# Optimization experiments

Hardware: AMD Instinct MI355X
Metric: run time of the kernel (lower is better)

Reference implementation:

```python
import jax, jax.numpy as jnp
import numpy as np

NEG_SLOPE = 0.2    # DenseGATConv attention leaky_relu slope (PyG default)
ACT_SLOPE = 0.01   # block activation LeakyReLU slope
HEADS = 3


def setup_inputs() -> dict:
    key = jax.random.key(0)
    B, N, D0, D1, D2, H = 512, 128, 128, 64, 64, HEADS
    ks = jax.random.split(key, 7)
    x = jax.random.normal(ks[0], (B * N, D0), jnp.float32)
    # equal-sized graphs: sorted graph ids, N atoms per graph
    batch_mask = jnp.repeat(jnp.arange(B, dtype=jnp.int32), N)
    s0 = 1.0 / np.sqrt(D0)
    s1 = 1.0 / np.sqrt(D1)
    s2 = 1.0 / np.sqrt(D2)
    W1 = jax.random.normal(ks[1], (D0, H * D1), jnp.float32) * s0
    att_src1 = jax.random.normal(ks[2], (H, D1), jnp.float32) * s1
    att_dst1 = jax.random.normal(ks[3], (H, D1), jnp.float32) * s1
    b1 = jnp.zeros((D1,), jnp.float32)
    W2 = jax.random.normal(ks[4], (D1, H * D2), jnp.float32) * s1
    att_src2 = jax.random.normal(ks[5], (H, D2), jnp.float32) * s2
    att_dst2 = jax.random.normal(ks[6], (H, D2), jnp.float32) * s2
    b2 = jnp.zeros((D2,), jnp.float32)
    return dict(x=x, batch_mask=batch_mask, W1=W1, att_src1=att_src1,
                att_dst1=att_dst1, b1=b1, W2=W2, att_src2=att_src2,
                att_dst2=att_dst2, b2=b2, batch_size=B, n_max=N)


def _dense_gat(x, adj, W, a_src, a_dst, b):
    # x: [B, N, Din], adj: [B, N, N] (self-loops already set). concat=False.
    B, N, _ = x.shape
    H, C = a_src.shape
    h = (x @ W).reshape(B, N, H, C)                       # lin (no bias)
    a_s = jnp.einsum('bnhc,hc->bnh', h, a_src)            # per-node src score
    a_d = jnp.einsum('bnhc,hc->bnh', h, a_dst)            # per-node dst score
    alpha = a_s[:, None, :, :] + a_d[:, :, None, :]       # [B, i, j, H]
    alpha = jax.nn.leaky_relu(alpha, NEG_SLOPE)
    alpha = jnp.where(adj[..., None] == 0, -jnp.inf, alpha)
    alpha = jax.nn.softmax(alpha, axis=2)                 # over source j
    out = jnp.einsum('bijh,bjhc->bihc', alpha, h)         # [B, N, H, C]
    return out.mean(axis=2) + b                           # concat=False -> head mean


def reference(x, batch_mask, W1, att_src1, att_dst1, b1,
              W2, att_src2, att_dst2, b2, batch_size, n_max):
    total, D0 = x.shape
    counts = jnp.bincount(batch_mask, length=batch_size)          # atoms per graph
    starts = jnp.cumsum(counts) - counts
    pos = jnp.arange(total) - starts[batch_mask]                  # slot within graph
    # to_dense_batch
    xd = jnp.zeros((batch_size, n_max, D0), x.dtype).at[batch_mask, pos].set(x)
    node_in = jnp.arange(n_max)[None, :] < counts[:, None]        # [B, N] valid mask
    # block adjacency: fully connected within each graph, diag zeroed...
    adj = (node_in[:, :, None] & node_in[:, None, :]).astype(x.dtype)
    # ...then DenseGATConv add_loop=True re-sets the full diagonal to 1
    adj = jnp.where(jnp.eye(n_max, dtype=bool), jnp.asarray(1.0, x.dtype), adj)
    h = _dense_gat(xd, adj, W1, att_src1, att_dst1, b1)
    h = jax.nn.leaky_relu(h, ACT_SLOPE)
    h = _dense_gat(h, adj, W2, att_src2, att_dst2, b2)
    h = jax.nn.leaky_relu(h, ACT_SLOPE)
    return jnp.sum(h, axis=1)                                     # sum pooling -> [B, D2]
```

## Files before the change

### kernel.cpp

```cpp
#include <hip/hip_runtime.h>
#include <stdint.h>

#define NROW 128
#define HCC  192

typedef __attribute__((ext_vector_type(8))) __bf16 bf16x8;
typedef __attribute__((ext_vector_type(4))) float  f32x4;

static __device__ __forceinline__ uint16_t f2bf(float f) {
    union { float f; uint32_t i; } v; v.f = f;
    uint32_t x = v.i;
    return (uint16_t)((x + 0x7FFFu + ((x >> 16) & 1u)) >> 16);
}
static __device__ __forceinline__ uint32_t pk2bf(float a, float b) {
    union { __bf16 h[2]; uint32_t u; } pk;
    pk.h[0] = (__bf16)a; pk.h[1] = (__bf16)b;
    return pk.u;
}

__global__ __launch_bounds__(256)
void prep_kernel(const float* __restrict__ W1, const float* __restrict__ W2,
                 uint16_t* __restrict__ wT1, uint16_t* __restrict__ wT2)
{
    int bid = blockIdx.x, t = threadIdx.x;
    if (bid < 96) {
        int idx = bid * 256 + t;
        int c = idx >> 7, k = idx & 127;
        wT1[c * 128 + k] = f2bf(W1[k * HCC + c]);
    } else {
        int idx = (bid - 96) * 256 + t;
        int c = idx >> 6, k = idx & 63;
        wT2[c * 64 + k] = f2bf(W2[k * HCC + c]);
    }
}

template<int K, bool POOL>
__global__ __launch_bounds__(512, 4)
void layer_kernel(const void* __restrict__ xin, const uint16_t* __restrict__ wTg,
                  const float* __restrict__ att_src, const float* __restrict__ att_dst,
                  const float* __restrict__ bias, void* __restrict__ outp)
{
    constexpr int XS = K + 8;
    constexpr int HS = 136;
    __shared__ __align__(16) uint16_t buf[HCC * HS];
    __shared__ __align__(16) float as_s[3 * 128];
    __shared__ __align__(16) float ad_s[3 * 128];
    __shared__ float attS[HCC], attD[HCC], bia[64], pool_s[8 * 64];

    uint16_t* wTl = buf;
    uint16_t* hT  = buf;

    const int b = blockIdx.x, t = threadIdx.x;
    const int w = t >> 6, l = t & 63, lr = l & 15, lg = l >> 4;
    const int i0 = w * 16;

    bf16x8 afr[K / 32];
    float4 raw[K == 128 ? 8 : 1][2];
    if (K == 128) {
        const float* xg = (const float*)xin + ((long)b * NROW + i0 + lr) * 128;
#pragma unroll
        for (int q = 0; q < 4; ++q) {
            raw[q][0] = *(const float4*)(xg + q * 32 + lg * 8);
            raw[q][1] = *(const float4*)(xg + q * 32 + lg * 8 + 4);
        }
    } else {
        const uint16_t* xg = (const uint16_t*)xin + ((long)b * NROW + i0 + lr) * 64;
#pragma unroll
        for (int q = 0; q < 2; ++q)
            afr[q] = *(const bf16x8*)(xg + q * 32 + lg * 8);
    }

    {
        constexpr int CH = K / 8;
#pragma unroll
        for (int p = 0; p < HCC * CH / 512; ++p) {
            int idx = t + p * 512; int row = idx / CH; int c8 = (idx % CH) * 8;
            *(uint4*)&wTl[row * XS + c8] = *(const uint4*)(wTg + row * K + c8);
        }
    }
    if (t < HCC) attS[t] = att_src[t];
    else if (t < 2 * HCC) attD[t - HCC] = att_dst[t - HCC];
    else if (t < 2 * HCC + 64) bia[t - 2 * HCC] = bias[t - 2 * HCC];

    if (K == 128) {
#pragma unroll
        for (int q = 0; q < 4; ++q) {
            bf16x8 a;
            a[0] = (__bf16)raw[q][0].x; a[1] = (__bf16)raw[q][0].y;
            a[2] = (__bf16)raw[q][0].z; a[3] = (__bf16)raw[q][0].w;
            a[4] = (__bf16)raw[q][1].x; a[5] = (__bf16)raw[q][1].y;
            a[6] = (__bf16)raw[q][1].z; a[7] = (__bf16)raw[q][1].w;
            afr[q] = a;
        }
    }
    __syncthreads();

    f32x4 hacc[12];
#pragma unroll
    for (int f = 0; f < 12; ++f) hacc[f] = (f32x4){0.f, 0.f, 0.f, 0.f};
#pragma unroll
    for (int q = 0; q < K / 32; ++q) {
        bf16x8 af = afr[q];
#pragma unroll
        for (int f = 0; f < 12; ++f) {
            bf16x8 bf = *(const bf16x8*)&wTl[(f * 16 + lr) * XS + q * 32 + lg * 8];
            hacc[f] = __builtin_amdgcn_mfma_f32_16x16x32_bf16(af, bf, hacc[f], 0, 0, 0);
        }
    }
    __syncthreads();

    {
        float ps[12], pd[12];
#pragma unroll
        for (int q = 0; q < 12; ++q) { ps[q] = 0.f; pd[q] = 0.f; }
#pragma unroll
        for (int f = 0; f < 12; ++f) {
            int hd = f >> 2;
            float av = attS[f * 16 + lr], dv = attD[f * 16 + lr];
#pragma unroll
            for (int r = 0; r < 4; ++r) {
                float hv = hacc[f][r];
                ps[hd * 4 + r] += hv * av;
                pd[hd * 4 + r] += hv * dv;
            }
        }
#pragma unroll
        for (int off = 1; off < 16; off <<= 1)
#pragma unroll
            for (int q = 0; q < 12; ++q) {
                ps[q] += __shfl_xor(ps[q], off);
                pd[q] += __shfl_xor(pd[q], off);
            }
        if (lr == 0) {
#pragma unroll
            for (int hd = 0; hd < 3; ++hd)
#pragma unroll
                for (int r = 0; r < 4; ++r) {
                    as_s[hd * 128 + i0 + lg * 4 + r] = ps[hd * 4 + r];
                    ad_s[hd * 128 + i0 + lg * 4 + r] = pd[hd * 4 + r];
                }
        }
#pragma unroll
        for (int f = 0; f < 12; ++f) {
            uint2 pv = make_uint2(pk2bf(hacc[f][0], hacc[f][1]),
                                  pk2bf(hacc[f][2], hacc[f][3]));
            *(uint2*)&hT[(f * 16 + lr) * HS + i0 + lg * 4] = pv;
        }
    }
    __syncthreads();

    f32x4 oacc[4];
#pragma unroll
    for (int f = 0; f < 4; ++f) oacc[f] = (f32x4){0.f, 0.f, 0.f, 0.f};

    for (int hd = 0; hd < 3; ++hd) {
        float a0 = as_s[hd * 128 + l], a1 = as_s[hd * 128 + l + 64];
        float mx = fmaxf(a0, a1);
#pragma unroll
        for (int off = 1; off < 64; off <<= 1) mx = fmaxf(mx, __shfl_xor(mx, off));
        float ad = ad_s[hd * 128 + i0 + lr];
        float m0 = mx + ad;
        float mi = fmaxf(m0, 0.2f * m0);

        float e[4][8];
        float zp = 0.f;
#pragma unroll
        for (int q = 0; q < 4; ++q) {
            float4 s0 = *(const float4*)&as_s[hd * 128 + q * 32 + lg * 8];
            float4 s1 = *(const float4*)&as_s[hd * 128 + q * 32 + lg * 8 + 4];
            float sv[8] = {s0.x, s0.y, s0.z, s0.w, s1.x, s1.y, s1.z, s1.w};
#pragma unroll
            for (int m = 0; m < 8; ++m) {
                float tt = sv[m] + ad;
                tt = fmaxf(tt, 0.2f * tt);
                float ev = __expf(tt - mi);
                e[q][m] = ev; zp += ev;
            }
        }
        zp += __shfl_xor(zp, 16);
        zp += __shfl_xor(zp, 32);
        float inv = 1.0f / zp;
        bf16x8 ap[4];
#pragma unroll
        for (int q = 0; q < 4; ++q)
#pragma unroll
            for (int m = 0; m < 8; ++m) ap[q][m] = (__bf16)(e[q][m] * inv);
#pragma unroll
        for (int q = 0; q < 4; ++q)
#pragma unroll
            for (int f = 0; f < 4; ++f) {
                bf16x8 bf = *(const bf16x8*)&hT[(hd * 64 + f * 16 + lr) * HS + q * 32 + lg * 8];
                oacc[f] = __builtin_amdgcn_mfma_f32_16x16x32_bf16(ap[q], bf, oacc[f], 0, 0, 0);
            }
    }

    const float inv3 = 1.f / 3.f;
    if (!POOL) {
        uint16_t* x2 = (uint16_t*)outp + (long)b * NROW * 64;
#pragma unroll
        for (int f = 0; f < 4; ++f) {
            int c = f * 16 + lr;
            float bv = bia[c];
#pragma unroll
            for (int r = 0; r < 4; ++r) {
                int i = i0 + lg * 4 + r;
                float v = oacc[f][r] * inv3 + bv;
                v = fmaxf(v, 0.01f * v);
                x2[i * 64 + c] = f2bf(v);
            }
        }
    } else {
#pragma unroll
        for (int f = 0; f < 4; ++f) {
            int c = f * 16 + lr;
            float bv = bia[c];
            float s = 0.f;
#pragma unroll
            for (int r = 0; r < 4; ++r) {
                float v = oacc[f][r] * inv3 + bv;
                v = fmaxf(v, 0.01f * v);
                s += v;
            }
            s += __shfl_xor(s, 16);
            s += __shfl_xor(s, 32);
            if (lg == 0) pool_s[w * 64 + c] = s;
        }
        __syncthreads();
        if (t < 64) {
            float s = 0.f;
#pragma unroll
            for (int q = 0; q < 8; ++q) s += pool_s[q * 64 + t];
            ((float*)outp)[(long)b * 64 + t] = s;
        }
    }
}

extern "C" void kernel_launch(void* const* d_in, const int* in_sizes, int n_in,
                              void* d_out, int out_size, void* d_ws, size_t ws_size,
                              hipStream_t stream)
{
    const float* x   = (const float*)d_in[0];
    const float* W1  = (const float*)d_in[2];
    const float* as1 = (const float*)d_in[3];
    const float* ad1 = (const float*)d_in[4];
    const float* b1  = (const float*)d_in[5];
    const float* W2  = (const float*)d_in[6];
    const float* as2 = (const float*)d_in[7];
    const float* ad2 = (const float*)d_in[8];
    const float* b2  = (const float*)d_in[9];

    uint16_t* wT1 = (uint16_t*)d_ws;
    uint16_t* wT2 = wT1 + 192 * 128;
    uint16_t* x2  = wT2 + 192 * 64;

    prep_kernel<<<144, 256, 0, stream>>>(W1, W2, wT1, wT2);
    layer_kernel<128, false><<<512, 512, 0, stream>>>((const void*)x,  wT1, as1, ad1, b1, (void*)x2);
    layer_kernel<64,  true ><<<512, 512, 0, stream>>>((const void*)x2, wT2, as2, ad2, b2, d_out);
}
```

Baseline: 138.3 us.

## Fuse both GAT layers into one kernel keeping intermediate features in LDS

Merges the two per-layer kernels into a single kernel per graph. The layer-1 output stays in shared memory as bf16 and never makes a global round trip. Layer-2 weights are prefetched into registers during the layer-1 softmax. The per-head max reductions are also batched across heads. This removes one launch and the intermediate global write and read, at the cost of more register pressure and a longer single kernel.

```diff
diff --git a/kernel.cpp b/kernel.cpp
--- a/kernel.cpp
+++ b/kernel.cpp
@@ -12,10 +12,9 @@
     uint32_t x = v.i;
     return (uint16_t)((x + 0x7FFFu + ((x >> 16) & 1u)) >> 16);
 }
-static __device__ __forceinline__ uint32_t pk2bf(float a, float b) {
-    union { __bf16 h[2]; uint32_t u; } pk;
-    pk.h[0] = (__bf16)a; pk.h[1] = (__bf16)b;
-    return pk.u;
+static __device__ __forceinline__ uint16_t bfbits(float f) {
+    __bf16 h = (__bf16)f;
+    union { __bf16 h; uint16_t u; } c; c.h = h; return c.u;
 }
 
 __global__ __launch_bounds__(256)
@@ -34,132 +33,73 @@
     }
 }
 
-template<int K, bool POOL>
-__global__ __launch_bounds__(512, 4)
-void layer_kernel(const void* __restrict__ xin, const uint16_t* __restrict__ wTg,
-                  const float* __restrict__ att_src, const float* __restrict__ att_dst,
-                  const float* __restrict__ bias, void* __restrict__ outp)
-{
-    constexpr int XS = K + 8;
-    constexpr int HS = 136;
-    __shared__ __align__(16) uint16_t buf[HCC * HS];
-    __shared__ __align__(16) float as_s[3 * 128];
-    __shared__ __align__(16) float ad_s[3 * 128];
-    __shared__ float attS[HCC], attD[HCC], bia[64], pool_s[8 * 64];
-
-    uint16_t* wTl = buf;
-    uint16_t* hT  = buf;
-
-    const int b = blockIdx.x, t = threadIdx.x;
-    const int w = t >> 6, l = t & 63, lr = l & 15, lg = l >> 4;
-    const int i0 = w * 16;
-
-    bf16x8 afr[K / 32];
-    float4 raw[K == 128 ? 8 : 1][2];
-    if (K == 128) {
-        const float* xg = (const float*)xin + ((long)b * NROW + i0 + lr) * 128;
-#pragma unroll
-        for (int q = 0; q < 4; ++q) {
-            raw[q][0] = *(const float4*)(xg + q * 32 + lg * 8);
-            raw[q][1] = *(const float4*)(xg + q * 32 + lg * 8 + 4);
-        }
-    } else {
-        const uint16_t* xg = (const uint16_t*)xin + ((long)b * NROW + i0 + lr) * 64;
-#pragma unroll
-        for (int q = 0; q < 2; ++q)
-            afr[q] = *(const bf16x8*)(xg + q * 32 + lg * 8);
-    }
-
-    {
-        constexpr int CH = K / 8;
-#pragma unroll
-        for (int p = 0; p < HCC * CH / 512; ++p) {
-            int idx = t + p * 512; int row = idx / CH; int c8 = (idx % CH) * 8;
-            *(uint4*)&wTl[row * XS + c8] = *(const uint4*)(wTg + row * K + c8);
-        }
-    }
-    if (t < HCC) attS[t] = att_src[t];
-    else if (t < 2 * HCC) attD[t - HCC] = att_dst[t - HCC];
-    else if (t < 2 * HCC + 64) bia[t - 2 * HCC] = bias[t - 2 * HCC];
-
-    if (K == 128) {
-#pragma unroll
-        for (int q = 0; q < 4; ++q) {
-            bf16x8 a;
-            a[0] = (__bf16)raw[q][0].x; a[1] = (__bf16)raw[q][0].y;
-            a[2] = (__bf16)raw[q][0].z; a[3] = (__bf16)raw[q][0].w;
-            a[4] = (__bf16)raw[q][1].x; a[5] = (__bf16)raw[q][1].y;
-            a[6] = (__bf16)raw[q][1].z; a[7] = (__bf16)raw[q][1].w;
-            afr[q] = a;
-        }
-    }
-    __syncthreads();
-
-    f32x4 hacc[12];
-#pragma unroll
-    for (int f = 0; f < 12; ++f) hacc[f] = (f32x4){0.f, 0.f, 0.f, 0.f};
-#pragma unroll
-    for (int q = 0; q < K / 32; ++q) {
-        bf16x8 af = afr[q];
-#pragma unroll
-        for (int f = 0; f < 12; ++f) {
-            bf16x8 bf = *(const bf16x8*)&wTl[(f * 16 + lr) * XS + q * 32 + lg * 8];
-            hacc[f] = __builtin_amdgcn_mfma_f32_16x16x32_bf16(af, bf, hacc[f], 0, 0, 0);
-        }
-    }
-    __syncthreads();
-
-    {
-        float ps[12], pd[12];
-#pragma unroll
-        for (int q = 0; q < 12; ++q) { ps[q] = 0.f; pd[q] = 0.f; }
-#pragma unroll
-        for (int f = 0; f < 12; ++f) {
-            int hd = f >> 2;
-            float av = attS[f * 16 + lr], dv = attD[f * 16 + lr];
+#define HS 136
+#define S2 72
+
+static __device__ __forceinline__
+void scores_and_hT(const f32x4* hacc, const float* attS, const float* attD,
+                   uint16_t* hT, float* as_s, float* ad_s,
+                   int i0, int lr, int lg)
+{
+    float ps[12], pd[12];
+#pragma unroll
+    for (int q = 0; q < 12; ++q) { ps[q] = 0.f; pd[q] = 0.f; }
+#pragma unroll
+    for (int f = 0; f < 12; ++f) {
+        int hd = f >> 2;
+        float av = attS[f * 16 + lr], dv = attD[f * 16 + lr];
+#pragma unroll
+        for (int r = 0; r < 4; ++r) {
+            float hv = hacc[f][r];
+            ps[hd * 4 + r] += hv * av;
+            pd[hd * 4 + r] += hv * dv;
+        }
+    }
+#pragma unroll
+    for (int off = 1; off < 16; off <<= 1)
+#pragma unroll
+        for (int q = 0; q < 12; ++q) {
+            ps[q] += __shfl_xor(ps[q], off);
+            pd[q] += __shfl_xor(pd[q], off);
+        }
+    if (lr == 0) {
+#pragma unroll
+        for (int hd = 0; hd < 3; ++hd)
 #pragma unroll
             for (int r = 0; r < 4; ++r) {
-                float hv = hacc[f][r];
-                ps[hd * 4 + r] += hv * av;
-                pd[hd * 4 + r] += hv * dv;
-            }
-        }
-#pragma unroll
-        for (int off = 1; off < 16; off <<= 1)
-#pragma unroll
-            for (int q = 0; q < 12; ++q) {
-                ps[q] += __shfl_xor(ps[q], off);
-                pd[q] += __shfl_xor(pd[q], off);
-            }
-        if (lr == 0) {
-#pragma unroll
-            for (int hd = 0; hd < 3; ++hd)
-#pragma unroll
-                for (int r = 0; r < 4; ++r) {
-                    as_s[hd * 128 + i0 + lg * 4 + r] = ps[hd * 4 + r];
-                    ad_s[hd * 128 + i0 + lg * 4 + r] = pd[hd * 4 + r];
-                }
-        }
-#pragma unroll
-        for (int f = 0; f < 12; ++f) {
-            uint2 pv = make_uint2(pk2bf(hacc[f][0], hacc[f][1]),
-                                  pk2bf(hacc[f][2], hacc[f][3]));
-            *(uint2*)&hT[(f * 16 + lr) * HS + i0 + lg * 4] = pv;
-        }
-    }
-    __syncthreads();
-
-    f32x4 oacc[4];
+                as_s[hd * 128 + i0 + lg * 4 + r] = ps[hd * 4 + r];
+                ad_s[hd * 128 + i0 + lg * 4 + r] = pd[hd * 4 + r];
+            }
+    }
+#pragma unroll
+    for (int f = 0; f < 12; ++f) {
+        uint32_t p0 = (uint32_t)bfbits(hacc[f][0]) | ((uint32_t)bfbits(hacc[f][1]) << 16);
+        uint32_t p1 = (uint32_t)bfbits(hacc[f][2]) | ((uint32_t)bfbits(hacc[f][3]) << 16);
+        *(uint2*)&hT[(f * 16 + lr) * HS + i0 + lg * 4] = make_uint2(p0, p1);
+    }
+}
+
+static __device__ __forceinline__
+void softmax_pv(const uint16_t* hT, const float* as_s, const float* ad_s,
+                f32x4* oacc, int i0, int l, int lr, int lg)
+{
 #pragma unroll
     for (int f = 0; f < 4; ++f) oacc[f] = (f32x4){0.f, 0.f, 0.f, 0.f};
 
+    float mxh[3];
+#pragma unroll
     for (int hd = 0; hd < 3; ++hd) {
         float a0 = as_s[hd * 128 + l], a1 = as_s[hd * 128 + l + 64];
-        float mx = fmaxf(a0, a1);
-#pragma unroll
-        for (int off = 1; off < 64; off <<= 1) mx = fmaxf(mx, __shfl_xor(mx, off));
+        mxh[hd] = fmaxf(a0, a1);
+    }
+#pragma unroll
+    for (int off = 1; off < 64; off <<= 1)
+#pragma unroll
+        for (int hd = 0; hd < 3; ++hd) mxh[hd] = fmaxf(mxh[hd], __shfl_xor(mxh[hd], off));
+
+    for (int hd = 0; hd < 3; ++hd) {
         float ad = ad_s[hd * 128 + i0 + lr];
-        float m0 = mx + ad;
+        float m0 = mxh[hd] + ad;
         float mi = fmaxf(m0, 0.2f * m0);
 
         float e[4][8];
@@ -189,31 +129,138 @@
         for (int q = 0; q < 4; ++q)
 #pragma unroll
             for (int f = 0; f < 4; ++f) {
-                bf16x8 bf = *(const bf16x8*)&hT[(hd * 64 + f * 16 + lr) * HS + q * 32 + lg * 8];
-                oacc[f] = __builtin_amdgcn_mfma_f32_16x16x32_bf16(ap[q], bf, oacc[f], 0, 0, 0);
-            }
-    }
-
-    const float inv3 = 1.f / 3.f;
-    if (!POOL) {
-        uint16_t* x2 = (uint16_t*)outp + (long)b * NROW * 64;
+                bf16x8 bfv = *(const bf16x8*)&hT[(hd * 64 + f * 16 + lr) * HS + q * 32 + lg * 8];
+                oacc[f] = __builtin_amdgcn_mfma_f32_16x16x32_bf16(ap[q], bfv, oacc[f], 0, 0, 0);
+            }
+    }
+}
+
+__global__ __launch_bounds__(512, 4)
+void fused_kernel(const float* __restrict__ x,
+                  const uint16_t* __restrict__ wT1g, const uint16_t* __restrict__ wT2g,
+                  const float* __restrict__ as1g, const float* __restrict__ ad1g,
+                  const float* __restrict__ b1g,
+                  const float* __restrict__ as2g, const float* __restrict__ ad2g,
+                  const float* __restrict__ b2g,
+                  float* __restrict__ outp)
+{
+    __shared__ __align__(16) uint16_t buf[HCC * HS];
+    __shared__ __align__(16) float as_s[3 * 128];
+    __shared__ __align__(16) float ad_s[3 * 128];
+    __shared__ float attS[2][HCC], attD[2][HCC], bia[2][64];
+    __shared__ float pool_s[8 * 64];
+
+    uint16_t* wT1l = buf;
+    uint16_t* hT   = buf;
+    uint16_t* x2T  = buf;
+    uint16_t* wT2l = buf + 128 * S2;
+
+    const int b = blockIdx.x, t = threadIdx.x;
+    const int w = t >> 6, l = t & 63, lr = l & 15, lg = l >> 4;
+    const int i0 = w * 16;
+
+    bf16x8 afr[4];
+    {
+        const float* xg = x + ((long)b * NROW + i0 + lr) * 128;
+        float4 r0[4], r1[4];
+#pragma unroll
+        for (int q = 0; q < 4; ++q) {
+            r0[q] = *(const float4*)(xg + q * 32 + lg * 8);
+            r1[q] = *(const float4*)(xg + q * 32 + lg * 8 + 4);
+        }
+#pragma unroll
+        for (int q = 0; q < 4; ++q) {
+            bf16x8 a;
+            a[0] = (__bf16)r0[q].x; a[1] = (__bf16)r0[q].y;
+            a[2] = (__bf16)r0[q].z; a[3] = (__bf16)r0[q].w;
+            a[4] = (__bf16)r1[q].x; a[5] = (__bf16)r1[q].y;
+            a[6] = (__bf16)r1[q].z; a[7] = (__bf16)r1[q].w;
+            afr[q] = a;
+        }
+    }
+#pragma unroll
+    for (int p = 0; p < 6; ++p) {
+        int idx = t + p * 512; int row = idx >> 4; int c8 = (idx & 15) * 8;
+        *(uint4*)&wT1l[row * HS + c8] = *(const uint4*)(wT1g + row * 128 + c8);
+    }
+    if (t < 192)      { attS[0][t] = as1g[t]; attD[0][t] = ad1g[t]; }
+    else if (t < 384) { attS[1][t - 192] = as2g[t - 192]; attD[1][t - 192] = ad2g[t - 192]; }
+    else if (t < 448) bia[0][t - 384] = b1g[t - 384];
+    else              bia[1][t - 448] = b2g[t - 448];
+    __syncthreads();
+
+    f32x4 hacc[12];
+#pragma unroll
+    for (int f = 0; f < 12; ++f) hacc[f] = (f32x4){0.f, 0.f, 0.f, 0.f};
+#pragma unroll
+    for (int q = 0; q < 4; ++q) {
+#pragma unroll
+        for (int f = 0; f < 12; ++f) {
+            bf16x8 bfv = *(const bf16x8*)&wT1l[(f * 16 + lr) * HS + q * 32 + lg * 8];
+            hacc[f] = __builtin_amdgcn_mfma_f32_16x16x32_bf16(afr[q], bfv, hacc[f], 0, 0, 0);
+        }
+    }
+    __syncthreads();
+
+    scores_and_hT(hacc, attS[0], attD[0], hT, as_s, ad_s, i0, lr, lg);
+    __syncthreads();
+
+    uint4 wpre[3];
+#pragma unroll
+    for (int p = 0; p < 3; ++p) {
+        int idx = t + p * 512; int row = idx >> 3; int c8 = (idx & 7) * 8;
+        wpre[p] = *(const uint4*)(wT2g + row * 64 + c8);
+    }
+
+    f32x4 oacc[4];
+    softmax_pv(hT, as_s, ad_s, oacc, i0, l, lr, lg);
+    __syncthreads();
+
+    {
+        const float inv3 = 1.f / 3.f;
 #pragma unroll
         for (int f = 0; f < 4; ++f) {
             int c = f * 16 + lr;
-            float bv = bia[c];
+            float bv = bia[0][c];
 #pragma unroll
             for (int r = 0; r < 4; ++r) {
-                int i = i0 + lg * 4 + r;
                 float v = oacc[f][r] * inv3 + bv;
                 v = fmaxf(v, 0.01f * v);
-                x2[i * 64 + c] = f2bf(v);
-            }
-        }
-    } else {
+                x2T[(i0 + lg * 4 + r) * S2 + c] = bfbits(v);
+            }
+        }
+#pragma unroll
+        for (int p = 0; p < 3; ++p) {
+            int idx = t + p * 512; int row = idx >> 3; int c8 = (idx & 7) * 8;
+            *(uint4*)&wT2l[row * S2 + c8] = wpre[p];
+        }
+    }
+    __syncthreads();
+
+#pragma unroll
+    for (int f = 0; f < 12; ++f) hacc[f] = (f32x4){0.f, 0.f, 0.f, 0.f};
+#pragma unroll
+    for (int q = 0; q < 2; ++q) {
+        bf16x8 af = *(const bf16x8*)&x2T[(i0 + lr) * S2 + q * 32 + lg * 8];
+#pragma unroll
+        for (int f = 0; f < 12; ++f) {
+            bf16x8 bfv = *(const bf16x8*)&wT2l[(f * 16 + lr) * S2 + q * 32 + lg * 8];
+            hacc[f] = __builtin_amdgcn_mfma_f32_16x16x32_bf16(af, bfv, hacc[f], 0, 0, 0);
+        }
+    }
+    __syncthreads();
+
+    scores_and_hT(hacc, attS[1], attD[1], hT, as_s, ad_s, i0, lr, lg);
+    __syncthreads();
+
+    softmax_pv(hT, as_s, ad_s, oacc, i0, l, lr, lg);
+
+    {
+        const float inv3 = 1.f / 3.f;
 #pragma unroll
         for (int f = 0; f < 4; ++f) {
             int c = f * 16 + lr;
-            float bv = bia[c];
+            float bv = bia[1][c];
             float s = 0.f;
 #pragma unroll
             for (int r = 0; r < 4; ++r) {
@@ -225,13 +272,13 @@
             s += __shfl_xor(s, 32);
             if (lg == 0) pool_s[w * 64 + c] = s;
         }
-        __syncthreads();
-        if (t < 64) {
-            float s = 0.f;
-#pragma unroll
-            for (int q = 0; q < 8; ++q) s += pool_s[q * 64 + t];
-            ((float*)outp)[(long)b * 64 + t] = s;
-        }
+    }
+    __syncthreads();
+    if (t < 64) {
+        float s = 0.f;
+#pragma unroll
+        for (int q = 0; q < 8; ++q) s += pool_s[q * 64 + t];
+        outp[(long)b * 64 + t] = s;
     }
 }
 
@@ -251,9 +298,8 @@
 
     uint16_t* wT1 = (uint16_t*)d_ws;
     uint16_t* wT2 = wT1 + 192 * 128;
-    uint16_t* x2  = wT2 + 192 * 64;
 
     prep_kernel<<<144, 256, 0, stream>>>(W1, W2, wT1, wT2);
-    layer_kernel<128, false><<<512, 512, 0, stream>>>((const void*)x,  wT1, as1, ad1, b1, (void*)x2);
-    layer_kernel<64,  true ><<<512, 512, 0, stream>>>((const void*)x2, wT2, as2, ad2, b2, d_out);
-}
+    fused_kernel<<<512, 512, 0, stream>>>(x, wT1, wT2, as1, ad1, b1, as2, ad2, b2,
+                                          (float*)d_out);
+}
```

Measured after the change: 131.7 us. 1.05x faster.
